# Performance work log

Hardware: AMD Instinct MI355X
Metric: run time of the kernel (lower is better)

The kernel has to match this reference:

```python
import jax, jax.numpy as jnp
import numpy as np

B, IN_CH, N, DIM, PH, HID, K = 4, 128, 2048, 256, 64, 1024, 16
EPS = 1e-5


def conv1(x, w, b):
    # 1x1 Conv1d: x (B,C,N), w (O,C) -> (B,O,N)
    return jnp.einsum('oc,bcn->bon', w, x) + b[None, :, None]


def conv2(x, w, b):
    # 1x1 Conv2d: x (B,C,N,K), w (O,C) -> (B,O,N,K)
    return jnp.einsum('oc,bcnk->bonk', w, x) + b[None, :, None, None]


def bn2(x, g, beta, mean, var):
    # eval-mode BatchNorm2d over channel dim of (B,C,N,K)
    scale = g * jax.lax.rsqrt(var + EPS)
    return x * scale[None, :, None, None] + (beta - mean * scale)[None, :, None, None]


def query_knn(pos, k):
    # pos: (B,3,N). Returns (B,N,K) indices of k nearest neighbors (incl. self).
    p = jnp.transpose(pos, (0, 2, 1))                     # (B,N,3)
    sq = jnp.sum(p * p, axis=-1)                          # (B,N)
    dist = sq[:, :, None] + sq[:, None, :] - 2.0 * jnp.einsum('bnc,bmc->bnm', p, p)
    _, idx = jax.lax.top_k(-dist, k)                      # smallest distances first
    return idx


def group(feat, idx):
    # feat: (B,C,N), idx: (B,N,K) -> (B,C,N,K) where out[b,c,i,k]=feat[b,c,idx[b,i,k]]
    b, c, n = feat.shape
    k = idx.shape[-1]
    ib = jnp.broadcast_to(idx.reshape(b, 1, n * k), (b, c, n * k))
    return jnp.take_along_axis(feat, ib, axis=2).reshape(b, c, n, k)


def setup_inputs() -> dict:
    key = jax.random.key(0)
    ks = jax.random.split(key, 12)
    s = 0.02
    return {
        'x': jax.random.normal(ks[0], (B, IN_CH, N), jnp.float32),
        'pos': jax.random.normal(ks[1], (B, 3, N), jnp.float32),
        'ls_w': jax.random.normal(ks[2], (DIM, IN_CH), jnp.float32) * s,
        'ls_b': jnp.zeros((DIM,), jnp.float32),
        'kw': jax.random.normal(ks[3], (DIM, DIM), jnp.float32) * s,
        'kb': jnp.zeros((DIM,), jnp.float32),
        'qw': jax.random.normal(ks[4], (DIM, DIM), jnp.float32) * s,
        'qb': jnp.zeros((DIM,), jnp.float32),
        'vw': jax.random.normal(ks[5], (DIM, DIM), jnp.float32) * s,
        'vb': jnp.zeros((DIM,), jnp.float32),
        'pw1': jax.random.normal(ks[6], (PH, 3), jnp.float32) * s,
        'pb1': jnp.zeros((PH,), jnp.float32),
        'pg': jnp.ones((PH,), jnp.float32),
        'pbeta': jnp.zeros((PH,), jnp.float32),
        'pmean': jnp.zeros((PH,), jnp.float32),
        'pvar': jnp.ones((PH,), jnp.float32),
        'pw2': jax.random.normal(ks[7], (DIM, PH), jnp.float32) * s,
        'pb2': jnp.zeros((DIM,), jnp.float32),
        'aw1': jax.random.normal(ks[8], (HID, DIM), jnp.float32) * s,
        'ab1': jnp.zeros((HID,), jnp.float32),
        'ag': jnp.ones((HID,), jnp.float32),
        'abeta': jnp.zeros((HID,), jnp.float32),
        'amean': jnp.zeros((HID,), jnp.float32),
        'avar': jnp.ones((HID,), jnp.float32),
        'aw2': jax.random.normal(ks[9], (DIM, HID), jnp.float32) * s,
        'ab2': jnp.zeros((DIM,), jnp.float32),
        'lw': jax.random.normal(ks[10], (IN_CH, DIM), jnp.float32) * s,
        'lb': jnp.zeros((IN_CH,), jnp.float32),
    }


def reference(x, pos, ls_w, ls_b, kw, kb, qw, qb, vw, vb,
              pw1, pb1, pg, pbeta, pmean, pvar, pw2, pb2,
              aw1, ab1, ag, abeta, amean, avar, aw2, ab2, lw, lb):
    identity = x
    h = conv1(x, ls_w, ls_b)                              # (B,DIM,N)
    idx = query_knn(pos, K)                               # (B,N,K) int32
    key_f = group(conv1(h, kw, kb), idx)                  # (B,DIM,N,K)
    value = conv1(h, vw, vb)                              # (B,DIM,N)
    query = conv1(h, qw, qb)                              # (B,DIM,N)
    qk_rel = query[:, :, :, None] - key_f                 # (B,DIM,N,K)
    pos_rel = pos[:, :, :, None] - group(pos, idx)        # (B,3,N,K)
    pe = conv2(jax.nn.relu(bn2(conv2(pos_rel, pw1, pb1), pg, pbeta, pmean, pvar)), pw2, pb2)
    attn = conv2(jax.nn.relu(bn2(conv2(qk_rel + pe, aw1, ab1), ag, abeta, amean, avar)), aw2, ab2)
    attn = jax.nn.softmax(attn, axis=-1)                  # softmax over K
    val_g = group(value, idx) + pe                        # (B,DIM,N,K)
    agg = jnp.sum(attn * val_g, axis=-1)                  # (B,DIM,N)
    y = conv1(agg, lw, lb)                                # (B,IN_CH,N)
    return y + identity
```

## Files before the change

### kernel.cpp

```cpp
#include <hip/hip_runtime.h>
#include <hip/hip_bf16.h>
#include <math.h>

#define B_    4
#define CIN   128
#define NPTS  2048
#define DIM   256
#define PH    64
#define HIDN  1024
#define KNN_  16
#define BN    (B_*NPTS)
#define CC    (BN*KNN_)
#define EPS_  1e-5f

typedef __bf16 bf16;
typedef __bf16 bf16x8 __attribute__((ext_vector_type(8)));
typedef __bf16 bf16x4 __attribute__((ext_vector_type(4)));
typedef float  f32x4  __attribute__((ext_vector_type(4)));

#define KNN_END   2048
#define PREP_CNT  2245
#define PREP_END  (KNN_END + PREP_CNT)
#define TR_END    (PREP_END + 128)
#define FOLD_END  (TR_END + 192)

__global__ __launch_bounds__(256) void combo_kernel(
    const float* __restrict__ pos, int* __restrict__ idx_out,
    const float* __restrict__ x, bf16* __restrict__ xT,
    const float* __restrict__ ls_w, const float* __restrict__ ls_b,
    const float* __restrict__ qw, const float* __restrict__ kw,
    const float* __restrict__ vw,
    const float* __restrict__ qb, const float* __restrict__ kb,
    const float* __restrict__ vb,
    const float* __restrict__ pw2,  const float* __restrict__ aw1,
    const float* __restrict__ aw2,  const float* __restrict__ lw,
    const float* __restrict__ pb1,  const float* __restrict__ pg,
    const float* __restrict__ pbeta,const float* __restrict__ pmean,
    const float* __restrict__ pvar,
    const float* __restrict__ ab1,  const float* __restrict__ ag,
    const float* __restrict__ abeta,const float* __restrict__ amean,
    const float* __restrict__ avar,
    bf16* pw2b, bf16* aw1b, bf16* aw2b, bf16* lwb,
    float* pe_scale, float* pe_shift, float* at_scale, float* at_shift,
    bf16* wfold, float* bfold)
{
  __shared__ __align__(16) char smem[33280];
  const int bid = blockIdx.x;
  const int tid = threadIdx.x;

  if (bid < KNN_END) {
    float* px = (float*)smem;
    float* py = px + NPTS;
    float* pz = py + NPTS;
    const int lane = tid & 63, wave = tid >> 6;
    const int q = bid * 4 + wave;
    const int b = q >> 11;
    const int n = q & (NPTS - 1);
    const float* p = pos + (long)b * 3 * NPTS;
    for (int j = tid; j < NPTS; j += 256) {
      px[j] = p[j]; py[j] = p[NPTS + j]; pz[j] = p[2 * NPTS + j];
    }
    __syncthreads();
    float qx = px[n], qy = py[n], qz = pz[n];
    float qs = qx * qx + qy * qy + qz * qz;
    float d[32];
#pragma unroll
    for (int j = 0; j < 32; ++j) {
      int pt = j * 64 + lane;
      float xx = px[pt], yy = py[pt], zz = pz[pt];
      float s2 = xx * xx + yy * yy + zz * zz;
      float dt = qx * xx + qy * yy + qz * zz;
      d[j] = qs + s2 - 2.f * dt;
    }
    for (int r = 0; r < KNN_; ++r) {
      float bv = 1e30f; int bj = 0;
#pragma unroll
      for (int j = 0; j < 32; ++j)
        if (d[j] < bv) { bv = d[j]; bj = j; }
      int bi = bj * 64 + lane;
#pragma unroll
      for (int off = 32; off >= 1; off >>= 1) {
        float ov = __shfl_xor(bv, off);
        int   oi = __shfl_xor(bi, off);
        if (ov < bv || (ov == bv && oi < bi)) { bv = ov; bi = oi; }
      }
      if (lane == 0) idx_out[(long)q * KNN_ + r] = bi;
#pragma unroll
      for (int j = 0; j < 32; ++j)
        if (bi == j * 64 + lane) d[j] = 1e30f;
    }
    return;
  }

  if (bid < PREP_END) {
    long e = (long)(bid - KNN_END) * 256 + tid;
    if (e < 16384)  { pw2b[e] = (bf16)pw2[e]; return; } e -= 16384;
    if (e < 262144) { aw1b[e] = (bf16)aw1[e]; return; } e -= 262144;
    if (e < 262144) { aw2b[e] = (bf16)aw2[e]; return; } e -= 262144;
    if (e < 32768)  { lwb[e]  = (bf16)lw[e];  return; } e -= 32768;
    if (e < 64) {
      float sc = pg[e] * rsqrtf(pvar[e] + EPS_);
      pe_scale[e] = sc;
      pe_shift[e] = sc * pb1[e] + pbeta[e] - pmean[e] * sc;
      return;
    } e -= 64;
    if (e < 1024) {
      float sc = ag[e] * rsqrtf(avar[e] + EPS_);
      at_scale[e] = sc;
      at_shift[e] = sc * ab1[e] + abeta[e] - amean[e] * sc;
    }
    return;
  }

  if (bid < TR_END) {
    float (*tile)[65] = (float(*)[65])smem;
    const int tb = bid - PREP_END;
    const int b = tb >> 5;
    const int n0 = (tb & 31) * 64;
    const float* xb = x + (long)b * CIN * NPTS;
#pragma unroll
    for (int it = 0; it < 32; ++it) {
      int row = it * 4 + (tid >> 6);
      int n = tid & 63;
      tile[row][n] = xb[(long)row * NPTS + n0 + n];
    }
    __syncthreads();
#pragma unroll
    for (int it = 0; it < 4; ++it) {
      int c = it * 256 + tid;
      int n = c >> 4;
      int ch0 = (c & 15) * 8;
      bf16x8 v;
#pragma unroll
      for (int j = 0; j < 8; ++j) v[j] = (bf16)tile[ch0 + j][n];
      *(bf16x8*)&xT[((long)b * NPTS + n0 + n) * CIN + ch0] = v;
    }
    return;
  }

  {
    const int lane = tid & 63, wave = tid >> 6;
    const int o = (bid - TR_END) * 4 + wave;
    const float* wsrc; const float* bsrc; int oo;
    if (o < 256)      { wsrc = qw + (long)o * DIM;        bsrc = qb; oo = o; }
    else if (o < 512) { wsrc = kw + (long)(o - 256) * DIM; bsrc = kb; oo = o - 256; }
    else              { wsrc = vw + (long)(o - 512) * DIM; bsrc = vb; oo = o - 512; }
    const int c0 = lane, c1 = lane + 64;
    float acc0 = 0.f, acc1 = 0.f, accb = 0.f;
    for (int dd = 0; dd < DIM; ++dd) {
      float w = wsrc[dd];
      acc0 += w * ls_w[(long)dd * CIN + c0];
      acc1 += w * ls_w[(long)dd * CIN + c1];
      accb += w * ls_b[dd];
    }
    wfold[(long)o * CIN + c0] = (bf16)acc0;
    wfold[(long)o * CIN + c1] = (bf16)acc1;
    if (lane == 0) bfold[o] = accb + bsrc[oo];
  }
}

template<int KD, bool OBF16>
__global__ __launch_bounds__(256) void gemmT_kernel(
    const bf16* __restrict__ inT, const bf16* __restrict__ Wb,
    const float* __restrict__ bias, void* __restrict__ outp, int O)
{
  const int tid = threadIdx.x;
  const int lane = tid & 63, wave = tid >> 6;
  const int row16 = lane & 15, grp = lane >> 4;
  const long i0 = (long)blockIdx.x * 64 + (wave & 1) * 32;
  const long o0 = (long)blockIdx.y * 64 + (wave >> 1) * 32;
  f32x4 acc[2][2] = {};
  const bf16* a0p = inT + (i0 + row16) * KD + grp * 8;
  const bf16* a1p = a0p + 16 * KD;
  const bf16* b0p = Wb + (o0 + row16) * KD + grp * 8;
  const bf16* b1p = b0p + 16 * KD;
#pragma unroll
  for (int ks = 0; ks < KD / 32; ++ks) {
    bf16x8 a0 = *(const bf16x8*)(a0p + ks * 32);
    bf16x8 a1 = *(const bf16x8*)(a1p + ks * 32);
    bf16x8 b0 = *(const bf16x8*)(b0p + ks * 32);
    bf16x8 b1 = *(const bf16x8*)(b1p + ks * 32);
    acc[0][0] = __builtin_amdgcn_mfma_f32_16x16x32_bf16(a0, b0, acc[0][0], 0, 0, 0);
    acc[0][1] = __builtin_amdgcn_mfma_f32_16x16x32_bf16(a0, b1, acc[0][1], 0, 0, 0);
    acc[1][0] = __builtin_amdgcn_mfma_f32_16x16x32_bf16(a1, b0, acc[1][0], 0, 0, 0);
    acc[1][1] = __builtin_amdgcn_mfma_f32_16x16x32_bf16(a1, b1, acc[1][1], 0, 0, 0);
  }
#pragma unroll
  for (int ot = 0; ot < 2; ++ot) {
    long o = o0 + ot * 16 + row16;
    float bv = bias[o];
#pragma unroll
    for (int it = 0; it < 2; ++it) {
#pragma unroll
      for (int r = 0; r < 4; ++r) {
        long i = i0 + it * 16 + grp * 4 + r;
        float v = acc[it][ot][r] + bv;
        if (OBF16) ((bf16*)outp)[i * O + o] = (bf16)v;
        else       ((float*)outp)[i * O + o] = v;
      }
    }
  }
}

__global__ __launch_bounds__(512, 4) void attn_fused_kernel(
    const bf16* __restrict__ qkvT, const float* __restrict__ pos,
    const int* __restrict__ idx, const float* __restrict__ pw1,
    const float* __restrict__ pe_scale, const float* __restrict__ pe_shift,
    const bf16* __restrict__ pw2b, const float* __restrict__ pb2,
    const bf16* __restrict__ aw1b, const bf16* __restrict__ aw2b,
    const float* __restrict__ at_scale, const float* __restrict__ at_shift,
    const float* __restrict__ ab2, bf16* __restrict__ aggT)
{
  __shared__ __align__(16) bf16 u_lds[64][264];
  __shared__ __align__(16) bf16 tbuf[64 * 136];
  __shared__ float rel_lds[64][4];
  __shared__ int   idx_lds[64];
  bf16 (*t_lds)[136]  = (bf16(*)[136])tbuf;
  bf16 (*hid_lds)[72] = (bf16(*)[72])tbuf;

  const int tid = threadIdx.x;
  const int lane = tid & 63, wave = tid >> 6;
  const int row16 = lane & 15, grp = lane >> 4;
  const long c0 = (long)blockIdx.x * 64;
  const int bn0 = blockIdx.x * 4;
  const int b = bn0 >> 11;
  const float* pB = pos + (long)b * 3 * NPTS;
  const int os = wave * 32;

  if (tid < 64) {
    int nb = idx[c0 + tid];
    idx_lds[tid] = nb;
    int n = (bn0 + (tid >> 4)) & (NPTS - 1);
    rel_lds[tid][0] = pB[n] - pB[nb];
    rel_lds[tid][1] = pB[NPTS + n] - pB[NPTS + nb];
    rel_lds[tid][2] = pB[2 * NPTS + n] - pB[2 * NPTS + nb];
  }
#pragma unroll
  for (int it = 0; it < 4; ++it) {
    int id = it * 512 + tid;
    int col = id >> 5, ch16 = id & 31;
    int nb = idx[c0 + col];
    *(bf16x8*)&u_lds[col][ch16 * 8] =
        *(const bf16x8*)(qkvT + ((long)b * NPTS + nb) * 768 + 256 + ch16 * 8);
  }
  __syncthreads();

  {
    int c = tid & 63, jq = tid >> 6;
    float rx = rel_lds[c][0], ry = rel_lds[c][1], rz = rel_lds[c][2];
#pragma unroll
    for (int jj = 0; jj < 8; ++jj) {
      int j = jq * 8 + jj;
      float v = pw1[j * 3] * rx + pw1[j * 3 + 1] * ry + pw1[j * 3 + 2] * rz;
      v = pe_scale[j] * v + pe_shift[j];
      hid_lds[c][j] = (bf16)fmaxf(v, 0.f);
    }
  }
  __syncthreads();

  f32x4 accpe[4][2] = {};
#pragma unroll
  for (int ks = 0; ks < 2; ++ks) {
    bf16x8 ah[4];
#pragma unroll
    for (int ct = 0; ct < 4; ++ct)
      ah[ct] = *(const bf16x8*)&hid_lds[ct * 16 + row16][ks * 32 + grp * 8];
#pragma unroll
    for (int ot = 0; ot < 2; ++ot) {
      bf16x8 bw = *(const bf16x8*)(pw2b + (long)(os + ot * 16 + row16) * PH + ks * 32 + grp * 8);
#pragma unroll
      for (int ct = 0; ct < 4; ++ct)
        accpe[ct][ot] = __builtin_amdgcn_mfma_f32_16x16x32_bf16(ah[ct], bw, accpe[ct][ot], 0, 0, 0);
    }
  }

  bf16x4 pe_bf[4][2];
#pragma unroll
  for (int ot = 0; ot < 2; ++ot) {
    int o = os + ot * 16 + row16;
    float pb2v = pb2[o];
#pragma unroll
    for (int ct = 0; ct < 4; ++ct) {
      float qv = (float)qkvT[(long)(bn0 + ct) * 768 + o];
#pragma unroll
      for (int r = 0; r < 4; ++r) {
        int c = ct * 16 + grp * 4 + r;
        float pev = accpe[ct][ot][r] + pb2v;
        float kv = (float)u_lds[c][o];
        u_lds[c][o] = (bf16)(qv - kv + pev);
        pe_bf[ct][ot][r] = (bf16)pev;
      }
    }
  }
  __syncthreads();

  const int hs16 = wave * 16;
  f32x4 acc2[4][2] = {};
  for (int jc = 0; jc < 8; ++jc) {
    const int hg = jc * 128 + hs16;
    f32x4 acc1[4] = {};
#pragma unroll
    for (int ks = 0; ks < 8; ++ks) {
      bf16x8 bu[4];
#pragma unroll
      for (int ct = 0; ct < 4; ++ct)
        bu[ct] = *(const bf16x8*)&u_lds[ct * 16 + row16][ks * 32 + grp * 8];
      bf16x8 aw = *(const bf16x8*)(aw1b + (long)(hg + row16) * DIM + ks * 32 + grp * 8);
#pragma unroll
      for (int ct = 0; ct < 4; ++ct)
        acc1[ct] = __builtin_amdgcn_mfma_f32_16x16x32_bf16(aw, bu[ct], acc1[ct], 0, 0, 0);
    }
    {
      f32x4 sc4 = *(const f32x4*)&at_scale[hg + grp * 4];
      f32x4 sh4 = *(const f32x4*)&at_shift[hg + grp * 4];
#pragma unroll
      for (int ct = 0; ct < 4; ++ct) {
        bf16x4 pk;
#pragma unroll
        for (int r = 0; r < 4; ++r) {
          float v = sc4[r] * acc1[ct][r] + sh4[r];
          pk[r] = (bf16)fmaxf(v, 0.f);
        }
        *(bf16x4*)&t_lds[ct * 16 + row16][hs16 + grp * 4] = pk;
      }
    }
    __syncthreads();
#pragma unroll
    for (int ks2 = 0; ks2 < 4; ++ks2) {
      bf16x8 a2[4], b2;
#pragma unroll
      for (int ct = 0; ct < 4; ++ct)
        a2[ct] = *(const bf16x8*)&t_lds[ct * 16 + row16][ks2 * 32 + grp * 8];
#pragma unroll
      for (int ot = 0; ot < 2; ++ot) {
        b2 = *(const bf16x8*)(aw2b + (long)(os + ot * 16 + row16) * HIDN + jc * 128 + ks2 * 32 + grp * 8);
#pragma unroll
        for (int ct = 0; ct < 4; ++ct)
          acc2[ct][ot] = __builtin_amdgcn_mfma_f32_16x16x32_bf16(a2[ct], b2, acc2[ct][ot], 0, 0, 0);
      }
    }
    __syncthreads();
  }

#pragma unroll
  for (int ct = 0; ct < 4; ++ct) {
#pragma unroll
    for (int ot = 0; ot < 2; ++ot) {
      int o = os + ot * 16 + row16;
      float ab = ab2[o];
      float l[4];
      float m = -1e30f;
#pragma unroll
      for (int r = 0; r < 4; ++r) {
        l[r] = acc2[ct][ot][r] + ab;
        m = fmaxf(m, l[r]);
      }
      m = fmaxf(m, __shfl_xor(m, 16));
      m = fmaxf(m, __shfl_xor(m, 32));
      float s = 0.f;
#pragma unroll
      for (int r = 0; r < 4; ++r) { l[r] = __expf(l[r] - m); s += l[r]; }
      s += __shfl_xor(s, 16);
      s += __shfl_xor(s, 32);
      float inv = 1.f / s;
      float agg = 0.f;
#pragma unroll
      for (int r = 0; r < 4; ++r) {
        int c = ct * 16 + grp * 4 + r;
        int nb = idx_lds[c];
        float vv = (float)qkvT[((long)b * NPTS + nb) * 768 + 512 + o];
        agg += l[r] * (vv + (float)pe_bf[ct][ot][r]);
      }
      agg *= inv;
      agg += __shfl_xor(agg, 16);
      agg += __shfl_xor(agg, 32);
      if (grp == 0) aggT[(long)(bn0 + ct) * DIM + o] = (bf16)agg;
    }
  }
}

__global__ __launch_bounds__(256) void final_kernel(
    const bf16* __restrict__ aggT, const bf16* __restrict__ lwb,
    const float* __restrict__ lb, const float* __restrict__ x,
    float* __restrict__ out)
{
  const int tid = threadIdx.x;
  const int lane = tid & 63, wave = tid >> 6;
  const int row16 = lane & 15, grp = lane >> 4;
  const long i0 = (long)blockIdx.x * 64 + (wave & 1) * 32;
  const int o0 = blockIdx.y * 64 + (wave >> 1) * 32;
  f32x4 acc[2][2] = {};
  const bf16* a0p = aggT + (i0 + row16) * DIM + grp * 8;
  const bf16* a1p = a0p + 16 * DIM;
  const bf16* b0p = lwb + (long)(o0 + row16) * DIM + grp * 8;
  const bf16* b1p = b0p + 16 * DIM;
#pragma unroll
  for (int ks = 0; ks < 8; ++ks) {
    bf16x8 a0 = *(const bf16x8*)(a0p + ks * 32);
    bf16x8 a1 = *(const bf16x8*)(a1p + ks * 32);
    bf16x8 b0 = *(const bf16x8*)(b0p + ks * 32);
    bf16x8 b1 = *(const bf16x8*)(b1p + ks * 32);
    acc[0][0] = __builtin_amdgcn_mfma_f32_16x16x32_bf16(a0, b0, acc[0][0], 0, 0, 0);
    acc[0][1] = __builtin_amdgcn_mfma_f32_16x16x32_bf16(a0, b1, acc[0][1], 0, 0, 0);
    acc[1][0] = __builtin_amdgcn_mfma_f32_16x16x32_bf16(a1, b0, acc[1][0], 0, 0, 0);
    acc[1][1] = __builtin_amdgcn_mfma_f32_16x16x32_bf16(a1, b1, acc[1][1], 0, 0, 0);
  }
#pragma unroll
  for (int ot = 0; ot < 2; ++ot) {
    int o = o0 + ot * 16 + row16;
    float bv = lb[o];
#pragma unroll
    for (int it = 0; it < 2; ++it) {
#pragma unroll
      for (int r = 0; r < 4; ++r) {
        long i = i0 + it * 16 + grp * 4 + r;
        int bb = (int)(i >> 11);
        int n = (int)(i & (NPTS - 1));
        long off = ((long)bb * CIN + o) * NPTS + n;
        out[off] = acc[it][ot][r] + bv + x[off];
      }
    }
  }
}

extern "C" void kernel_launch(void* const* d_in, const int* in_sizes, int n_in,
                              void* d_out, int out_size, void* d_ws, size_t ws_size,
                              hipStream_t stream)
{
  const float* x     = (const float*)d_in[0];
  const float* pos   = (const float*)d_in[1];
  const float* ls_w  = (const float*)d_in[2];
  const float* ls_b  = (const float*)d_in[3];
  const float* kw    = (const float*)d_in[4];
  const float* kb    = (const float*)d_in[5];
  const float* qw    = (const float*)d_in[6];
  const float* qb    = (const float*)d_in[7];
  const float* vw    = (const float*)d_in[8];
  const float* vb    = (const float*)d_in[9];
  const float* pw1   = (const float*)d_in[10];
  const float* pb1   = (const float*)d_in[11];
  const float* pg    = (const float*)d_in[12];
  const float* pbeta = (const float*)d_in[13];
  const float* pmean = (const float*)d_in[14];
  const float* pvar  = (const float*)d_in[15];
  const float* pw2   = (const float*)d_in[16];
  const float* pb2   = (const float*)d_in[17];
  const float* aw1   = (const float*)d_in[18];
  const float* ab1   = (const float*)d_in[19];
  const float* ag    = (const float*)d_in[20];
  const float* abeta = (const float*)d_in[21];
  const float* amean = (const float*)d_in[22];
  const float* avar  = (const float*)d_in[23];
  const float* aw2   = (const float*)d_in[24];
  const float* ab2   = (const float*)d_in[25];
  const float* lw    = (const float*)d_in[26];
  const float* lb    = (const float*)d_in[27];

  char* ws = (char*)d_ws;
  size_t off = 0;
  auto alloc = [&](size_t bytes) -> void* {
    void* p = ws + off;
    off = (off + bytes + 255) & ~(size_t)255;
    return p;
  };

  bf16* pw2b  = (bf16*)alloc(16384 * 2);
  bf16* aw1b  = (bf16*)alloc(262144 * 2);
  bf16* aw2b  = (bf16*)alloc(262144 * 2);
  bf16* lwb   = (bf16*)alloc(32768 * 2);
  float* pe_scale = (float*)alloc(64 * 4);
  float* pe_shift = (float*)alloc(64 * 4);
  float* at_scale = (float*)alloc(1024 * 4);
  float* at_shift = (float*)alloc(1024 * 4);
  bf16* wfold = (bf16*)alloc(98304 * 2);
  float* bfold = (float*)alloc(768 * 4);
  int*  idx  = (int*)alloc((size_t)CC * 4);
  bf16* xT   = (bf16*)alloc((size_t)BN * CIN * 2);
  bf16* qkvT = (bf16*)alloc((size_t)BN * 768 * 2);
  bf16* aggT = (bf16*)alloc((size_t)BN * DIM * 2);

  combo_kernel<<<dim3(FOLD_END), 256, 0, stream>>>(
      pos, idx, x, xT,
      ls_w, ls_b, qw, kw, vw, qb, kb, vb,
      pw2, aw1, aw2, lw,
      pb1, pg, pbeta, pmean, pvar, ab1, ag, abeta, amean, avar,
      pw2b, aw1b, aw2b, lwb,
      pe_scale, pe_shift, at_scale, at_shift,
      wfold, bfold);

  gemmT_kernel<128, true><<<dim3(BN / 64, 768 / 64), 256, 0, stream>>>(xT, wfold, bfold, qkvT, 768);

  attn_fused_kernel<<<dim3(CC / 64), 512, 0, stream>>>(
      qkvT, pos, idx, pw1, pe_scale, pe_shift, pw2b, pb2,
      aw1b, aw2b, at_scale, at_shift, ab2, aggT);

  final_kernel<<<dim3(BN / 64, CIN / 64), 256, 0, stream>>>(aggT, lwb, lb, x, (float*)d_out);
}
```

Measured before the change: 464.4 us.

## Fuse final linear projection and residual into attention kernel epilogue

```diff
diff --git a/kernel.cpp b/kernel.cpp
--- a/kernel.cpp
+++ b/kernel.cpp
@@ -209,7 +209,9 @@
     const bf16* __restrict__ pw2b, const float* __restrict__ pb2,
     const bf16* __restrict__ aw1b, const bf16* __restrict__ aw2b,
     const float* __restrict__ at_scale, const float* __restrict__ at_shift,
-    const float* __restrict__ ab2, bf16* __restrict__ aggT)
+    const float* __restrict__ ab2,
+    const bf16* __restrict__ lwb, const float* __restrict__ lb,
+    const float* __restrict__ x, float* __restrict__ out)
 {
   __shared__ __align__(16) bf16 u_lds[64][264];
   __shared__ __align__(16) bf16 tbuf[64 * 136];
@@ -217,6 +219,7 @@
   __shared__ int   idx_lds[64];
   bf16 (*t_lds)[136]  = (bf16(*)[136])tbuf;
   bf16 (*hid_lds)[72] = (bf16(*)[72])tbuf;
+  float* agg_f = (float*)tbuf;
 
   const int tid = threadIdx.x;
   const int lane = tid & 63, wave = tid >> 6;
@@ -374,52 +377,26 @@
       agg *= inv;
       agg += __shfl_xor(agg, 16);
       agg += __shfl_xor(agg, 32);
-      if (grp == 0) aggT[(long)(bn0 + ct) * DIM + o] = (bf16)agg;
-    }
-  }
-}
-
-__global__ __launch_bounds__(256) void final_kernel(
-    const bf16* __restrict__ aggT, const bf16* __restrict__ lwb,
-    const float* __restrict__ lb, const float* __restrict__ x,
-    float* __restrict__ out)
-{
-  const int tid = threadIdx.x;
-  const int lane = tid & 63, wave = tid >> 6;
-  const int row16 = lane & 15, grp = lane >> 4;
-  const long i0 = (long)blockIdx.x * 64 + (wave & 1) * 32;
-  const int o0 = blockIdx.y * 64 + (wave >> 1) * 32;
-  f32x4 acc[2][2] = {};
-  const bf16* a0p = aggT + (i0 + row16) * DIM + grp * 8;
-  const bf16* a1p = a0p + 16 * DIM;
-  const bf16* b0p = lwb + (long)(o0 + row16) * DIM + grp * 8;
-  const bf16* b1p = b0p + 16 * DIM;
-#pragma unroll
-  for (int ks = 0; ks < 8; ++ks) {
-    bf16x8 a0 = *(const bf16x8*)(a0p + ks * 32);
-    bf16x8 a1 = *(const bf16x8*)(a1p + ks * 32);
-    bf16x8 b0 = *(const bf16x8*)(b0p + ks * 32);
-    bf16x8 b1 = *(const bf16x8*)(b1p + ks * 32);
-    acc[0][0] = __builtin_amdgcn_mfma_f32_16x16x32_bf16(a0, b0, acc[0][0], 0, 0, 0);
-    acc[0][1] = __builtin_amdgcn_mfma_f32_16x16x32_bf16(a0, b1, acc[0][1], 0, 0, 0);
-    acc[1][0] = __builtin_amdgcn_mfma_f32_16x16x32_bf16(a1, b0, acc[1][0], 0, 0, 0);
-    acc[1][1] = __builtin_amdgcn_mfma_f32_16x16x32_bf16(a1, b1, acc[1][1], 0, 0, 0);
-  }
-#pragma unroll
-  for (int ot = 0; ot < 2; ++ot) {
-    int o = o0 + ot * 16 + row16;
-    float bv = lb[o];
-#pragma unroll
-    for (int it = 0; it < 2; ++it) {
-#pragma unroll
-      for (int r = 0; r < 4; ++r) {
-        long i = i0 + it * 16 + grp * 4 + r;
-        int bb = (int)(i >> 11);
-        int n = (int)(i & (NPTS - 1));
-        long off = ((long)bb * CIN + o) * NPTS + n;
-        out[off] = acc[it][ot][r] + bv + x[off];
-      }
-    }
+      if (grp == 0) agg_f[o * 4 + ct] = agg;
+    }
+  }
+  __syncthreads();
+
+  {
+    const int o = tid >> 2;
+    const int pt = tid & 3;
+    const int n = (bn0 + pt) & (NPTS - 1);
+    const bf16* lrow = lwb + (long)o * DIM;
+    float acc = lb[o];
+#pragma unroll
+    for (int d8 = 0; d8 < 32; ++d8) {
+      bf16x8 w8 = *(const bf16x8*)(lrow + d8 * 8);
+#pragma unroll
+      for (int j = 0; j < 8; ++j)
+        acc += (float)w8[j] * agg_f[(d8 * 8 + j) * 4 + pt];
+    }
+    long off = ((long)b * CIN + o) * NPTS + n;
+    out[off] = acc + x[off];
   }
 }
 
@@ -477,7 +454,6 @@
   int*  idx  = (int*)alloc((size_t)CC * 4);
   bf16* xT   = (bf16*)alloc((size_t)BN * CIN * 2);
   bf16* qkvT = (bf16*)alloc((size_t)BN * 768 * 2);
-  bf16* aggT = (bf16*)alloc((size_t)BN * DIM * 2);
 
   combo_kernel<<<dim3(FOLD_END), 256, 0, stream>>>(
       pos, idx, x, xT,
@@ -492,7 +468,6 @@
 
   attn_fused_kernel<<<dim3(CC / 64), 512, 0, stream>>>(
       qkvT, pos, idx, pw1, pe_scale, pe_shift, pw2b, pb2,
-      aw1b, aw2b, at_scale, at_shift, ab2, aggT);
-
-  final_kernel<<<dim3(BN / 64, CIN / 64), 256, 0, stream>>>(aggT, lwb, lb, x, (float*)d_out);
+      aw1b, aw2b, at_scale, at_shift, ab2,
+      lwb, lb, x, (float*)d_out);
 }
```

New measurement: 469.7 us. No clear change (+1.1%).
